# Kernel optimization log

Measured on AMD Instinct MI355X. Metric: run time of the kernel, lower is better.

The kernel has to match this reference:

```python
import jax, jax.numpy as jnp
import numpy as np

NEG_SLOPE = 0.2
EPS = 1e-16


def setup_inputs() -> dict:
    key = jax.random.key(0)
    k1, k2, k3, k4, k5 = jax.random.split(key, 5)
    N, E, F_IN, H, C = 100000, 1600000, 128, 4, 32
    x = jax.random.normal(k1, (N, F_IN), dtype=jnp.float32)
    edge_index = jax.random.randint(k2, (2, E), 0, N, dtype=jnp.int64)
    W = jax.random.normal(k3, (F_IN, H * C), dtype=jnp.float32) * (1.0 / np.sqrt(F_IN))
    att_src = jax.random.normal(k4, (H, C), dtype=jnp.float32) * 0.1
    att_dst = jax.random.normal(k5, (H, C), dtype=jnp.float32) * 0.1
    bias = jnp.zeros((H * C,), dtype=jnp.float32)
    return {"x": x, "edge_index": edge_index, "W": W, "att_src": att_src,
            "att_dst": att_dst, "bias": bias}


def reference(x, edge_index, W, att_src, att_dst, bias):
    N = x.shape[0]
    H, C = att_src.shape
    # PyG GATConv default: add self-loops
    loops = jnp.arange(N, dtype=edge_index.dtype)
    src = jnp.concatenate([edge_index[0], loops])  # [E+N]
    dst = jnp.concatenate([edge_index[1], loops])  # [E+N]

    h = (x @ W).reshape(N, H, C)                  # [N,H,C]
    a_src = jnp.einsum('nhc,hc->nh', h, att_src)  # [N,H]
    a_dst = jnp.einsum('nhc,hc->nh', h, att_dst)  # [N,H]

    e = a_src[src] + a_dst[dst]                   # [E',H]
    e = jax.nn.leaky_relu(e, NEG_SLOPE)

    # segment softmax over destination nodes (numerically stable)
    m = jax.ops.segment_max(e, dst, num_segments=N)      # [N,H]
    p = jnp.exp(e - m[dst])                               # [E',H]
    s = jax.ops.segment_sum(p, dst, num_segments=N)       # [N,H]
    alpha = p / (s[dst] + EPS)                             # [E',H]

    msg = h[src] * alpha[:, :, None]                       # [E',H,C]
    out = jax.ops.segment_sum(msg, dst, num_segments=N)   # [N,H,C]
    return out.reshape(N, H * C) + bias
```

## Files before the change

kernel.cpp:

```cpp
#include <hip/hip_runtime.h>
#include <stdint.h>


#define SLOT 64
#define CNTS 16
#define BCNS 16
#define BCAP 1536
#define MAXB 2048
#define KCH  8192
#define PST  68

typedef __attribute__((ext_vector_type(8))) _Float16 h8;
typedef __attribute__((ext_vector_type(4))) float    f4x;
typedef __attribute__((ext_vector_type(2))) unsigned u32x2;

__device__ __forceinline__ float b2f(unsigned short u) {
    union { unsigned int i; float f; } v; v.i = ((unsigned int)u) << 16; return v.f;
}
__device__ __forceinline__ unsigned short f2b(float f) {
    union { float f; unsigned int i; } v; v.f = f;
    unsigned int i = v.i;
    unsigned int r = (i + 0x7FFFu + ((i >> 16) & 1u)) >> 16;
    return (unsigned short)r;
}
__device__ __forceinline__ unsigned short f2h(float f) {
    union { _Float16 h; unsigned short u; } v; v.h = (_Float16)f; return v.u;
}
__device__ __forceinline__ float h2f(unsigned short u) {
    union { _Float16 h; unsigned short u; } v; v.u = u; return (float)v.h;
}

__global__ void k_detect(const int* __restrict__ eidx, const unsigned int* __restrict__ xw,
                         int* flags) {
    __shared__ int nz, bf;
    if (threadIdx.x == 0) { nz = 0; bf = 0; }
    __syncthreads();
    int bad = 0;
    for (int i = threadIdx.x; i < 1024; i += 256)
        if (eidx[2 * i + 1] != 0) bad = 1;
    if (bad) atomicOr(&nz, 1);
    int hits = 0;
    for (int i = threadIdx.x; i < 4096; i += 256) {
        unsigned int e = (xw[i] >> 7) & 0xFFu;
        if (e >= 0x60u && e < 0xA0u) ++hits;
    }
    atomicAdd(&bf, hits);
    __syncthreads();
    if (threadIdx.x == 0) {
        flags[0] = (nz == 0) ? 1 : 0;
        flags[1] = (bf > 3072) ? 1 : 0;
    }
}

__device__ __forceinline__ int edge_at(const int* idx32, const long long* idx64,
                                       int is64, long long pos) {
    return is64 ? (int)idx64[pos] : idx32[pos];
}

__global__ void k_prep(const void* __restrict__ Wv, const void* __restrict__ asv,
                       const void* __restrict__ adv, const void* __restrict__ bv,
                       const int* __restrict__ flags,
                       _Float16* __restrict__ Wth, _Float16* __restrict__ Wtl,
                       float* __restrict__ attf , float* __restrict__ biasf ) {
    int isbf = flags[1];
    int tid = blockIdx.x * 256 + threadIdx.x;
    for (int i = tid; i < 16384; i += gridDim.x * 256) {
        int col = i >> 7, k = i & 127;
        float w = isbf ? b2f(((const unsigned short*)Wv)[k * 128 + col])
                       : ((const float*)Wv)[k * 128 + col];
        unsigned short hi = f2h(w);
        unsigned short lo = f2h(w - h2f(hi));
        ((unsigned short*)Wth)[i] = hi;
        ((unsigned short*)Wtl)[i] = lo;
    }
    if (blockIdx.x == 0) {
        for (int i = threadIdx.x; i < 128; i += 256) {
            attf[i]       = isbf ? b2f(((const unsigned short*)asv)[i]) : ((const float*)asv)[i];
            attf[128 + i] = isbf ? b2f(((const unsigned short*)adv)[i]) : ((const float*)adv)[i];
            biasf[i]      = isbf ? b2f(((const unsigned short*)bv)[i]) : ((const float*)bv)[i];
        }
    }
}

__global__ __launch_bounds__(256) void k_gemm_scatter(
    const void* __restrict__ xv,
    const _Float16* __restrict__ Wth, const _Float16* __restrict__ Wtl,
    const float* __restrict__ attf, const int* __restrict__ flags,
    unsigned short* __restrict__ hbf, float* __restrict__ asf,
    float* __restrict__ adf, int N,
    const int* __restrict__ idx32, const long long* __restrict__ idx64,
    int* __restrict__ bcnt, unsigned* __restrict__ bdat,
    int* __restrict__ cnt, int* __restrict__ esrc,
    int E, int Gg, int SB) {
    __shared__ unsigned short xsh[64 * 128];
    __shared__ unsigned short xsl[64 * 128];
    int tid = threadIdx.x;
    int bid = blockIdx.x;

    if (bid < SB) {
        int is64 = flags[0];
        int NBK = (N + 63) >> 6;
        long long e0 = (long long)bid * KCH;
        long long e1 = e0 + KCH; if (e1 > E) e1 = E;
        if (e0 >= E) return;

        if (NBK <= MAXB) {
            int wid = tid >> 6;
            int* h0 = (int*)xsh; int* h1 = h0 + MAXB;
            int* h2 = (int*)xsl; int* h3 = h2 + MAXB;
            int* hw = (wid == 0) ? h0 : (wid == 1) ? h1 : (wid == 2) ? h2 : h3;
            for (int i = tid; i < NBK; i += 256) { h0[i] = 0; h1[i] = 0; h2[i] = 0; h3[i] = 0; }
            __syncthreads();
            for (long long e = e0 + tid; e < e1; e += 256) {
                int d = is64 ? (int)idx64[(long long)E + e] : idx32[E + e];
                atomicAdd(&hw[d >> 6], 1);
            }
            __syncthreads();
            for (int b = tid; b < NBK; b += 256) {
                int c0 = h0[b], c1 = h1[b], c2 = h2[b], c3 = h3[b];
                int t = c0 + c1 + c2 + c3;
                int base = (t > 0) ? atomicAdd(&bcnt[(size_t)b * BCNS], t) : 0;
                h0[b] = base;
                h1[b] = base + c0;
                h2[b] = base + c0 + c1;
                h3[b] = base + c0 + c1 + c2;
            }
            __syncthreads();
            for (long long e = e0 + tid; e < e1; e += 256) {
                int d, s;
                if (is64) {
                    d = (int)idx64[(long long)E + e]; s = (int)idx64[e];
                } else {
                    d = idx32[E + e]; s = idx32[e];
                }
                int b = d >> 6;
                int p = atomicAdd(&hw[b], 1);
                if (p < BCAP)
                    bdat[(size_t)b * BCAP + p] = (unsigned)s | ((unsigned)(d & 63) << 26);
            }
        } else {
            for (long long e = e0 + tid; e < e1; e += 256) {
                int d = edge_at(idx32, idx64, is64, (long long)E + e);
                int s = edge_at(idx32, idx64, is64, e);
                int p = atomicAdd(&cnt[(size_t)d * CNTS], 1);
                if (p < SLOT) esrc[(size_t)d * SLOT + p] = s;
            }
        }
        return;
    }

    int rb = bid - SB;
    if (rb >= Gg) return;
    int r0 = rb * 64;
    int isbf = flags[1];
    int w = tid >> 6;
    int lane = tid & 63;
    int li = lane & 15;
    int g  = lane >> 4;
    int c0 = w * 32;

    h8 Bh[2][4], Bl[2][4];
#pragma unroll
    for (int t = 0; t < 2; ++t)
#pragma unroll
        for (int s = 0; s < 4; ++s) {
            size_t o = (size_t)(c0 + 16 * t + li) * 128 + 32 * s + 8 * g;
            Bh[t][s] = *(const h8*)(Wth + o);
            Bl[t][s] = *(const h8*)(Wtl + o);
        }

#pragma unroll
    for (int it = 0; it < 4; ++it) {
        int idx = it * 2048 + tid * 8;
        int r = idx >> 7, k = idx & 127;
        int gr = r0 + r; if (gr >= N) gr = N - 1;
        float v[8];
        if (isbf) {
            uint4 raw = *(const uint4*)((const unsigned short*)xv + (size_t)gr * 128 + k);
            v[0] = b2f((unsigned short)(raw.x & 0xFFFFu)); v[1] = b2f((unsigned short)(raw.x >> 16));
            v[2] = b2f((unsigned short)(raw.y & 0xFFFFu)); v[3] = b2f((unsigned short)(raw.y >> 16));
            v[4] = b2f((unsigned short)(raw.z & 0xFFFFu)); v[5] = b2f((unsigned short)(raw.z >> 16));
            v[6] = b2f((unsigned short)(raw.w & 0xFFFFu)); v[7] = b2f((unsigned short)(raw.w >> 16));
        } else {
            const float* xf = (const float*)xv;
            float4 a = *(const float4*)(xf + (size_t)gr * 128 + k);
            float4 b = *(const float4*)(xf + (size_t)gr * 128 + k + 4);
            v[0] = a.x; v[1] = a.y; v[2] = a.z; v[3] = a.w;
            v[4] = b.x; v[5] = b.y; v[6] = b.z; v[7] = b.w;
        }
        uint4 PH, PL;
        unsigned int ph[4], pl[4];
#pragma unroll
        for (int jj = 0; jj < 4; ++jj) {
            unsigned short h0 = f2h(v[2 * jj]), h1 = f2h(v[2 * jj + 1]);
            unsigned short l0 = f2h(v[2 * jj] - h2f(h0));
            unsigned short l1 = f2h(v[2 * jj + 1] - h2f(h1));
            ph[jj] = (unsigned int)h0 | ((unsigned int)h1 << 16);
            pl[jj] = (unsigned int)l0 | ((unsigned int)l1 << 16);
        }
        PH.x = ph[0]; PH.y = ph[1]; PH.z = ph[2]; PH.w = ph[3];
        PL.x = pl[0]; PL.y = pl[1]; PL.z = pl[2]; PL.w = pl[3];
        int off = r * 256 + ((2 * k) ^ ((r & 7) << 4));
        *(uint4*)((char*)xsh + off) = PH;
        *(uint4*)((char*)xsl + off) = PL;
    }
    __syncthreads();

    f4x acc[4][2];
#pragma unroll
    for (int m = 0; m < 4; ++m)
#pragma unroll
        for (int t = 0; t < 2; ++t) acc[m][t] = (f4x){0.f, 0.f, 0.f, 0.f};

#pragma unroll
    for (int s = 0; s < 4; ++s) {
#pragma unroll
        for (int m = 0; m < 4; ++m) {
            int row = 16 * m + li;
            int kb = (32 * s + 8 * g) * 2;
            int off = row * 256 + (kb ^ ((row & 7) << 4));
            h8 ah = *(const h8*)((const char*)xsh + off);
            h8 al = *(const h8*)((const char*)xsl + off);
#pragma unroll
            for (int t = 0; t < 2; ++t) {
                acc[m][t] = __builtin_amdgcn_mfma_f32_16x16x32_f16(ah, Bh[t][s], acc[m][t], 0, 0, 0);
                acc[m][t] = __builtin_amdgcn_mfma_f32_16x16x32_f16(al, Bh[t][s], acc[m][t], 0, 0, 0);
                acc[m][t] = __builtin_amdgcn_mfma_f32_16x16x32_f16(ah, Bl[t][s], acc[m][t], 0, 0, 0);
            }
        }
    }

    float at_s0 = attf[c0 + li],       at_s1 = attf[c0 + 16 + li];
    float at_d0 = attf[128 + c0 + li], at_d1 = attf[128 + c0 + 16 + li];
#pragma unroll
    for (int m = 0; m < 4; ++m) {
        float s1v[4], s2v[4];
#pragma unroll
        for (int j = 0; j < 4; ++j) {
            s1v[j] = acc[m][0][j] * at_s0 + acc[m][1][j] * at_s1;
            s2v[j] = acc[m][0][j] * at_d0 + acc[m][1][j] * at_d1;
        }
#pragma unroll
        for (int j = 0; j < 4; ++j) {
#pragma unroll
            for (int msk = 1; msk < 16; msk <<= 1) {
                s1v[j] += __shfl_xor(s1v[j], msk);
                s2v[j] += __shfl_xor(s2v[j], msk);
            }
        }
        if (li == 0) {
#pragma unroll
            for (int j = 0; j < 4; ++j) {
                int gr = r0 + 16 * m + 4 * g + j;
                if (gr < N) {
                    asf[(size_t)gr * 4 + w] = s1v[j];
                    adf[(size_t)gr * 4 + w] = s2v[j];
                }
            }
        }
    }

    __syncthreads();
#pragma unroll
    for (int m = 0; m < 4; ++m)
#pragma unroll
        for (int t = 0; t < 2; ++t)
#pragma unroll
            for (int j = 0; j < 4; ++j)
                xsh[(16 * m + 4 * g + j) * 128 + c0 + 16 * t + li] = f2b(acc[m][t][j]);
    __syncthreads();
#pragma unroll
    for (int it = 0; it < 4; ++it) {
        int u = it * 2048 + tid * 8;
        int r = u >> 7, k = u & 127;
        int gr = r0 + r;
        if (gr < N)
            *(uint4*)(hbf + (size_t)gr * 128 + k) = *(const uint4*)(xsh + u);
    }
}

template <int NB>
__device__ __forceinline__ void agg_node2(
    int n, int dl, int deg, int lane,
    const int lslot[64][SLOT], float* psh,
    const unsigned short* __restrict__ hbf,
    const float* __restrict__ asf, const float* __restrict__ adf,
    float a[4], float& invho) {
    int half = lane >> 5;
    int cl = lane & 31;
    int hd = cl >> 3;
    int sl = (lane == 0) ? n : ((lane <= deg) ? lslot[dl][lane - 1] : n);
    float4 av, adv;
    asm volatile("global_load_dwordx4 %0, %1, off"
                 : "=v"(av) : "v"((const void*)(asf + (size_t)sl * 4)));
    asm volatile("global_load_dwordx4 %0, %1, off"
                 : "=v"(adv) : "v"((const void*)(adf + (size_t)n * 4)));
    u32x2 vv[NB * 8];
#pragma unroll
    for (int k = 0; k < NB * 8; ++k) {
        int it = 2 * k + half;
        int s = (it == 0) ? n : ((it <= deg) ? lslot[dl][it - 1] : n);
        asm volatile("global_load_dwordx2 %0, %1, off"
                     : "=v"(vv[k]) : "v"((const void*)(hbf + (size_t)s * 128 + 4 * cl)));
    }
    asm volatile("s_waitcnt vmcnt(%0)" :: "n"(NB * 8));
    __builtin_amdgcn_sched_barrier(0);

    float p0 = 0.f, p1 = 0.f, p2 = 0.f, p3 = 0.f;
    if (lane <= deg) {
        float e0 = av.x + adv.x; e0 = fmaxf(e0, 0.2f * e0); p0 = __expf(e0);
        float e1 = av.y + adv.y; e1 = fmaxf(e1, 0.2f * e1); p1 = __expf(e1);
        float e2 = av.z + adv.z; e2 = fmaxf(e2, 0.2f * e2); p2 = __expf(e2);
        float e3 = av.w + adv.w; e3 = fmaxf(e3, 0.2f * e3); p3 = __expf(e3);
    }
    psh[0 * PST + lane] = p0; psh[1 * PST + lane] = p1;
    psh[2 * PST + lane] = p2; psh[3 * PST + lane] = p3;
    __builtin_amdgcn_wave_barrier();
    asm volatile("s_waitcnt lgkmcnt(0)" ::: "memory");
    __builtin_amdgcn_wave_barrier();

    float ps0 = p0, ps1 = p1, ps2 = p2, ps3 = p3;
#pragma unroll
    for (int m = 1; m < 64; m <<= 1) {
        ps0 += __shfl_xor(ps0, m);
        ps1 += __shfl_xor(ps1, m);
        ps2 += __shfl_xor(ps2, m);
        ps3 += __shfl_xor(ps3, m);
    }
    float den = hd == 0 ? ps0 : hd == 1 ? ps1 : hd == 2 ? ps2 : ps3;
    invho = 1.0f / (den + 1e-16f);

#pragma unroll
    for (int bi = 0; bi < NB; ++bi) {
        asm volatile("s_waitcnt vmcnt(%0)" :: "n"(8 * (NB - 1 - bi)));
        __builtin_amdgcn_sched_barrier(0);
#pragma unroll
        for (int k2 = 0; k2 < 8; ++k2) {
            int it = 2 * (bi * 8 + k2) + half;
            float q = psh[hd * PST + it];
            u32x2 v = vv[bi * 8 + k2];
            a[0] += q * b2f((unsigned short)v[0]);
            a[1] += q * b2f((unsigned short)(v[0] >> 16));
            a[2] += q * b2f((unsigned short)v[1]);
            a[3] += q * b2f((unsigned short)(v[1] >> 16));
        }
    }
}

__global__ __launch_bounds__(256) void k_bagg(
    const unsigned* __restrict__ bdat, const int* __restrict__ bcnt,
    const unsigned short* __restrict__ hbf,
    const float* __restrict__ asf, const float* __restrict__ adf,
    const int* __restrict__ idx32, const long long* __restrict__ idx64,
    const float* __restrict__ biasf, const int* __restrict__ flags,
    void* __restrict__ outv, int N, int E) {
    __shared__ int   lcnt[64];
    __shared__ int   lslot[64][SLOT];
    __shared__ float p_all[4][4 * PST];
    int b = blockIdx.x, tid = threadIdx.x;
    int wid = tid >> 6, lane = tid & 63, head = lane >> 4;

    if (tid < 64) lcnt[tid] = 0;
    __syncthreads();
    int mm = bcnt[(size_t)b * BCNS];
    int ovf = (mm > BCAP);
    if (mm > BCAP) mm = BCAP;
    for (int i = tid; i < mm; i += 256) {
        unsigned e = bdat[(size_t)b * BCAP + i];
        int dl = (int)(e >> 26);
        int p = atomicAdd(&lcnt[dl], 1);
        if (p < SLOT) lslot[dl][p] = (int)(e & 0x03FFFFFFu);
    }
    __syncthreads();

    int cl = lane & 31;
    float b0 = biasf[2 * lane], b1 = biasf[2 * lane + 1];
    float4 bq4 = *(const float4*)(biasf + 4 * cl);
    float* psh = p_all[wid];
    int isbf = flags[1];
    int is64 = flags[0];

    for (int u = 0; u < 16; ++u) {
        int dl = wid * 16 + u;
        int n = (b << 6) + dl;
        if (n >= N) break;
        int deg = lcnt[dl];
        bool fb = ovf || (deg > SLOT - 1);

        if (!fb && deg <= 31) {
            float a4[4] = {0.f, 0.f, 0.f, 0.f};
            float invh = 0.f;
            int nb = (deg + 16) >> 4;
            if (nb == 1) agg_node2<1>(n, dl, deg, lane, lslot, psh, hbf, asf, adf, a4, invh);
            else         agg_node2<2>(n, dl, deg, lane, lslot, psh, hbf, asf, adf, a4, invh);
#pragma unroll
            for (int c = 0; c < 4; ++c) a4[c] += __shfl_xor(a4[c], 32);
            float o0 = a4[0] * invh + bq4.x, o1 = a4[1] * invh + bq4.y;
            float o2 = a4[2] * invh + bq4.z, o3 = a4[3] * invh + bq4.w;
            if (lane < 32) {
                if (isbf) {
                    u32x2 pk;
                    pk[0] = (unsigned)f2b(o0) | ((unsigned)f2b(o1) << 16);
                    pk[1] = (unsigned)f2b(o2) | ((unsigned)f2b(o3) << 16);
                    *(u32x2*)((unsigned*)outv + (size_t)n * 64 + cl * 2) = pk;
                } else {
                    float4 f4v; f4v.x = o0; f4v.y = o1; f4v.z = o2; f4v.w = o3;
                    *(float4*)((float*)outv + (size_t)n * 128 + cl * 4) = f4v;
                }
            }
        } else if (!fb) {
            float a0 = 0.f, a1 = 0.f;
            float4 adv = *(const float4*)(adf + (size_t)n * 4);
            int sl = (lane == 0) ? n : ((lane <= deg) ? lslot[dl][lane - 1] : n);
            float4 av = *(const float4*)(asf + (size_t)sl * 4);
            float p0 = 0.f, p1 = 0.f, p2 = 0.f, p3 = 0.f;
            if (lane <= deg) {
                float e0 = av.x + adv.x; e0 = fmaxf(e0, 0.2f * e0); p0 = __expf(e0);
                float e1 = av.y + adv.y; e1 = fmaxf(e1, 0.2f * e1); p1 = __expf(e1);
                float e2 = av.z + adv.z; e2 = fmaxf(e2, 0.2f * e2); p2 = __expf(e2);
                float e3 = av.w + adv.w; e3 = fmaxf(e3, 0.2f * e3); p3 = __expf(e3);
            }
            psh[0 * PST + lane] = p0; psh[1 * PST + lane] = p1;
            psh[2 * PST + lane] = p2; psh[3 * PST + lane] = p3;
            __builtin_amdgcn_wave_barrier();
            asm volatile("s_waitcnt lgkmcnt(0)" ::: "memory");
            __builtin_amdgcn_wave_barrier();
            float ps0 = p0, ps1 = p1, ps2 = p2, ps3 = p3;
#pragma unroll
            for (int m = 1; m < 64; m <<= 1) {
                ps0 += __shfl_xor(ps0, m);
                ps1 += __shfl_xor(ps1, m);
                ps2 += __shfl_xor(ps2, m);
                ps3 += __shfl_xor(ps3, m);
            }
            float den = head == 0 ? ps0 : head == 1 ? ps1 : head == 2 ? ps2 : ps3;
            float invh = 1.0f / (den + 1e-16f);
            int nb = (deg + 8) >> 3;
            for (int bi = 0; bi < nb; ++bi) {
                unsigned vt[8];
#pragma unroll
                for (int k2 = 0; k2 < 8; ++k2) {
                    int it = bi * 8 + k2;
                    int s = (it == 0) ? n : ((it <= deg) ? lslot[dl][it - 1] : n);
                    vt[k2] = *(const unsigned int*)(hbf + (size_t)s * 128 + 2 * lane);
                }
#pragma unroll
                for (int k2 = 0; k2 < 8; ++k2) {
                    float q = psh[head * PST + bi * 8 + k2];
                    a0 += q * b2f((unsigned short)vt[k2]);
                    a1 += q * b2f((unsigned short)(vt[k2] >> 16));
                }
            }
            a0 = a0 * invh + b0;
            a1 = a1 * invh + b1;
            if (isbf) {
                unsigned int pk = (unsigned int)f2b(a0) | ((unsigned int)f2b(a1) << 16);
                ((unsigned int*)outv)[(size_t)n * 64 + lane] = pk;
            } else {
                float2 f2; f2.x = a0; f2.y = a1;
                *(float2*)((float*)outv + (size_t)n * 128 + 2 * lane) = f2;
            }
        } else {
            float a0 = 0.f, a1 = 0.f;
            float4 adv = *(const float4*)(adf + (size_t)n * 4);
            float adh = head == 0 ? adv.x : head == 1 ? adv.y : head == 2 ? adv.z : adv.w;
            float den = 0.f;
            {
                float ev = asf[(size_t)n * 4 + head] + adh; ev = fmaxf(ev, 0.2f * ev);
                float p = __expf(ev);
                unsigned int v = *(const unsigned int*)(hbf + (size_t)n * 128 + 2 * lane);
                den += p;
                a0 += p * b2f((unsigned short)v);
                a1 += p * b2f((unsigned short)(v >> 16));
            }
            for (int e = 0; e < E; ++e) {
                int d = edge_at(idx32, idx64, is64, (long long)E + e);
                if (d == n) {
                    int s = edge_at(idx32, idx64, is64, e);
                    float ev = asf[(size_t)s * 4 + head] + adh; ev = fmaxf(ev, 0.2f * ev);
                    float p = __expf(ev);
                    unsigned int v = *(const unsigned int*)(hbf + (size_t)s * 128 + 2 * lane);
                    den += p;
                    a0 += p * b2f((unsigned short)v);
                    a1 += p * b2f((unsigned short)(v >> 16));
                }
            }
            float invh = 1.0f / (den + 1e-16f);
            a0 = a0 * invh + b0;
            a1 = a1 * invh + b1;
            if (isbf) {
                unsigned int pk = (unsigned int)f2b(a0) | ((unsigned int)f2b(a1) << 16);
                ((unsigned int*)outv)[(size_t)n * 64 + lane] = pk;
            } else {
                float2 f2; f2.x = a0; f2.y = a1;
                *(float2*)((float*)outv + (size_t)n * 128 + 2 * lane) = f2;
            }
        }
        __builtin_amdgcn_wave_barrier();
    }
}

__global__ __launch_bounds__(256) void k_aggregate(
    const unsigned short* __restrict__ hbf,
    const float* __restrict__ asf, const float* __restrict__ adf,
    const int* __restrict__ cnt, const int* __restrict__ esrc,
    const int* __restrict__ idx32, const long long* __restrict__ idx64,
    const float* __restrict__ biasf, const int* __restrict__ flags,
    void* __restrict__ outv, int N, int E) {
    __shared__ float p_sh_all[4][SLOT * 4];
    __shared__ int   s_sh_all[4][SLOT];
    int wid = threadIdx.x >> 6;
    int lane = threadIdx.x & 63;
    int n = blockIdx.x * 4 + wid;
    if (n >= N) n = N - 1;
    float* p_sh = p_sh_all[wid];
    int*   s_sh = s_sh_all[wid];
    int head = lane >> 4;

    int deg = cnt[(size_t)n * CNTS];
    float4 adv = *(const float4*)(adf + (size_t)n * 4);
    bool fb = (deg > SLOT - 1);

    float p0 = 0.f, p1 = 0.f, p2 = 0.f, p3 = 0.f;
    if (!fb && lane <= deg) {
        int s = (lane == 0) ? n : esrc[(size_t)n * SLOT + lane - 1];
        float4 av = *(const float4*)(asf + (size_t)s * 4);
        float e0 = av.x + adv.x; e0 = fmaxf(e0, 0.2f * e0); p0 = __expf(e0);
        float e1 = av.y + adv.y; e1 = fmaxf(e1, 0.2f * e1); p1 = __expf(e1);
        float e2 = av.z + adv.z; e2 = fmaxf(e2, 0.2f * e2); p2 = __expf(e2);
        float e3 = av.w + adv.w; e3 = fmaxf(e3, 0.2f * e3); p3 = __expf(e3);
        s_sh[lane] = s;
        p_sh[lane * 4 + 0] = p0; p_sh[lane * 4 + 1] = p1;
        p_sh[lane * 4 + 2] = p2; p_sh[lane * 4 + 3] = p3;
    }
    __syncthreads();

    float b0 = biasf[2 * lane], b1 = biasf[2 * lane + 1];
    float a0 = 0.f, a1 = 0.f, invh;

    if (!fb) {
        float ps0 = p0, ps1 = p1, ps2 = p2, ps3 = p3;
#pragma unroll
        for (int m = 1; m < 64; m <<= 1) {
            ps0 += __shfl_xor(ps0, m);
            ps1 += __shfl_xor(ps1, m);
            ps2 += __shfl_xor(ps2, m);
            ps3 += __shfl_xor(ps3, m);
        }
        float den = head == 0 ? ps0 : head == 1 ? ps1 : head == 2 ? ps2 : ps3;
        invh = 1.0f / (den + 1e-16f);

        int tot = deg + 1;
        int i = 0;
        for (; i + 3 < tot; i += 4) {
            int s0 = s_sh[i], s1 = s_sh[i + 1], s2 = s_sh[i + 2], s3 = s_sh[i + 3];
            float q0 = p_sh[i * 4 + head],       q1 = p_sh[(i + 1) * 4 + head];
            float q2 = p_sh[(i + 2) * 4 + head], q3 = p_sh[(i + 3) * 4 + head];
            unsigned int v0 = *(const unsigned int*)(hbf + (size_t)s0 * 128 + 2 * lane);
            unsigned int v1 = *(const unsigned int*)(hbf + (size_t)s1 * 128 + 2 * lane);
            unsigned int v2 = *(const unsigned int*)(hbf + (size_t)s2 * 128 + 2 * lane);
            unsigned int v3 = *(const unsigned int*)(hbf + (size_t)s3 * 128 + 2 * lane);
            a0 += q0 * b2f((unsigned short)v0) + q1 * b2f((unsigned short)v1)
                + q2 * b2f((unsigned short)v2) + q3 * b2f((unsigned short)v3);
            a1 += q0 * b2f((unsigned short)(v0 >> 16)) + q1 * b2f((unsigned short)(v1 >> 16))
                + q2 * b2f((unsigned short)(v2 >> 16)) + q3 * b2f((unsigned short)(v3 >> 16));
        }
        for (; i < tot; ++i) {
            int s0 = s_sh[i];
            float q0 = p_sh[i * 4 + head];
            unsigned int v0 = *(const unsigned int*)(hbf + (size_t)s0 * 128 + 2 * lane);
            a0 += q0 * b2f((unsigned short)v0);
            a1 += q0 * b2f((unsigned short)(v0 >> 16));
        }
    } else {
        int is64 = flags[0];
        float adh = head == 0 ? adv.x : head == 1 ? adv.y : head == 2 ? adv.z : adv.w;
        float den = 0.f;
        {
            float ev = asf[(size_t)n * 4 + head] + adh; ev = fmaxf(ev, 0.2f * ev);
            float p = __expf(ev);
            unsigned int v = *(const unsigned int*)(hbf + (size_t)n * 128 + 2 * lane);
            den += p;
            a0 += p * b2f((unsigned short)v);
            a1 += p * b2f((unsigned short)(v >> 16));
        }
        for (int e = 0; e < E; ++e) {
            int d = edge_at(idx32, idx64, is64, (long long)E + e);
            if (d == n) {
                int s = edge_at(idx32, idx64, is64, e);
                float ev = asf[(size_t)s * 4 + head] + adh; ev = fmaxf(ev, 0.2f * ev);
                float p = __expf(ev);
                unsigned int v = *(const unsigned int*)(hbf + (size_t)s * 128 + 2 * lane);
                den += p;
                a0 += p * b2f((unsigned short)v);
                a1 += p * b2f((unsigned short)(v >> 16));
            }
        }
        invh = 1.0f / (den + 1e-16f);
    }

    a0 = a0 * invh + b0;
    a1 = a1 * invh + b1;
    if (flags[1]) {
        unsigned int pk = (unsigned int)f2b(a0) | ((unsigned int)f2b(a1) << 16);
        ((unsigned int*)outv)[(size_t)n * 64 + lane] = pk;
    } else {
        float2 f2; f2.x = a0; f2.y = a1;
        *(float2*)((float*)outv + (size_t)n * 128 + 2 * lane) = f2;
    }
}

extern "C" void kernel_launch(void* const* d_in, const int* in_sizes, int n_in,
                              void* d_out, int out_size, void* d_ws, size_t ws_size,
                              hipStream_t stream) {
    const void*      xv    = d_in[0];
    const int*       idx32 = (const int*)d_in[1];
    const long long* idx64 = (const long long*)d_in[1];

    int N = in_sizes[0] / 128;
    int E = in_sizes[1] / 2;

    char* ws = (char*)d_ws;
    size_t o = 0;
    auto alloc = [&](size_t bytes) {
        size_t r = o; o += (bytes + 255) & ~(size_t)255; return r;
    };
    unsigned short* hbf = (unsigned short*)(ws + alloc((size_t)N * 128 * 2));
    _Float16* Wth = (_Float16*)(ws + alloc(16384 * 2));
    _Float16* Wtl = (_Float16*)(ws + alloc(16384 * 2));
    float* attf  = (float*)(ws + alloc(256 * 4));
    float* biasf = (float*)(ws + alloc(128 * 4));
    float* asf   = (float*)(ws + alloc((size_t)N * 4 * 4));
    float* adf   = (float*)(ws + alloc((size_t)N * 4 * 4));
    int* cnt     = (int*)(ws + alloc((size_t)N * CNTS * 4));
    int* flags   = (int*)(ws + alloc(256));
    int* esrc    = (int*)(ws + alloc((size_t)N * SLOT * 4));
    int NBK = (N + 63) >> 6;
    int* bcnt      = (int*)(ws + alloc((size_t)NBK * BCNS * 4));
    unsigned* bdat = (unsigned*)(ws + alloc((size_t)NBK * BCAP * 4));

    int Gg = (N + 63) / 64;
    int SB = (E + KCH - 1) / KCH;
    int NB = SB + Gg;

    k_detect<<<1, 256, 0, stream>>>(idx32, (const unsigned int*)xv, flags);
    k_prep<<<16, 256, 0, stream>>>(d_in[2], d_in[3], d_in[4], d_in[5], flags, Wth, Wtl, attf, biasf);
    if (NBK <= MAXB) {
        hipMemsetAsync(bcnt, 0, (size_t)NBK * BCNS * 4, stream);
        k_gemm_scatter<<<NB, 256, 0, stream>>>(xv, Wth, Wtl, attf, flags, hbf, asf, adf, N,
                                               idx32, idx64, bcnt, bdat, cnt, esrc, E, Gg, SB);
        k_bagg<<<NBK, 256, 0, stream>>>(bdat, bcnt, hbf, asf, adf, idx32, idx64,
                                        biasf, flags, d_out, N, E);
    } else {
        hipMemsetAsync(cnt, 0, (size_t)N * CNTS * 4, stream);
        k_gemm_scatter<<<NB, 256, 0, stream>>>(xv, Wth, Wtl, attf, flags, hbf, asf, adf, N,
                                               idx32, idx64, bcnt, bdat, cnt, esrc, E, Gg, SB);
        k_aggregate<<<(N + 3) / 4, 256, 0, stream>>>(hbf, asf, adf, cnt, esrc, idx32, idx64,
                                                     biasf, flags, d_out, N, E);
    }
}
```

Measured before the change: 254.0 us.

## Fold detection and bucket-count clearing into prep kernel; split aggregation blocks in two

Merges the dtype/index detection kernel and the bucket-counter memset into the prep kernel, removing two launches from the stream. Each prep block recomputes the bf16 heuristic locally so it does not need a cross-block flag read. The bucket aggregation kernel now launches two blocks per 64-node bucket, each handling 32 destination nodes, which doubles parallelism. The cost is that both blocks redundantly read and bin the whole bucket's edge list into shared memory.

```diff
diff --git a/kernel.cpp b/kernel.cpp
--- a/kernel.cpp
+++ b/kernel.cpp
@@ -30,28 +30,6 @@
     union { _Float16 h; unsigned short u; } v; v.u = u; return (float)v.h;
 }
 
-__global__ void k_detect(const int* __restrict__ eidx, const unsigned int* __restrict__ xw,
-                         int* flags) {
-    __shared__ int nz, bf;
-    if (threadIdx.x == 0) { nz = 0; bf = 0; }
-    __syncthreads();
-    int bad = 0;
-    for (int i = threadIdx.x; i < 1024; i += 256)
-        if (eidx[2 * i + 1] != 0) bad = 1;
-    if (bad) atomicOr(&nz, 1);
-    int hits = 0;
-    for (int i = threadIdx.x; i < 4096; i += 256) {
-        unsigned int e = (xw[i] >> 7) & 0xFFu;
-        if (e >= 0x60u && e < 0xA0u) ++hits;
-    }
-    atomicAdd(&bf, hits);
-    __syncthreads();
-    if (threadIdx.x == 0) {
-        flags[0] = (nz == 0) ? 1 : 0;
-        flags[1] = (bf > 3072) ? 1 : 0;
-    }
-}
-
 __device__ __forceinline__ int edge_at(const int* idx32, const long long* idx64,
                                        int is64, long long pos) {
     return is64 ? (int)idx64[pos] : idx32[pos];
@@ -59,12 +37,37 @@
 
 __global__ void k_prep(const void* __restrict__ Wv, const void* __restrict__ asv,
                        const void* __restrict__ adv, const void* __restrict__ bv,
-                       const int* __restrict__ flags,
+                       const int* __restrict__ eidx, const unsigned int* __restrict__ xw,
+                       int* __restrict__ flags,
                        _Float16* __restrict__ Wth, _Float16* __restrict__ Wtl,
-                       float* __restrict__ attf , float* __restrict__ biasf ) {
-    int isbf = flags[1];
-    int tid = blockIdx.x * 256 + threadIdx.x;
-    for (int i = tid; i < 16384; i += gridDim.x * 256) {
+                       float* __restrict__ attf , float* __restrict__ biasf ,
+                       int* __restrict__ bcnt, int nbcnt ) {
+    __shared__ int nz, bf;
+    int tid = threadIdx.x;
+    if (tid == 0) { nz = 0; bf = 0; }
+    __syncthreads();
+    int hits = 0;
+    for (int i = tid; i < 4096; i += 256) {
+        unsigned int e = (xw[i] >> 7) & 0xFFu;
+        if (e >= 0x60u && e < 0xA0u) ++hits;
+    }
+    atomicAdd(&bf, hits);
+    if (blockIdx.x == 0) {
+        int bad = 0;
+        for (int i = tid; i < 1024; i += 256)
+            if (eidx[2 * i + 1] != 0) bad = 1;
+        if (bad) atomicOr(&nz, 1);
+    }
+    __syncthreads();
+    int isbf = (bf > 3072) ? 1 : 0;
+    if (blockIdx.x == 0 && tid == 0) {
+        flags[0] = (nz == 0) ? 1 : 0;
+        flags[1] = isbf;
+    }
+    for (int i = blockIdx.x * 256 + tid; i < nbcnt; i += gridDim.x * 256)
+        bcnt[i] = 0;
+    int gtid = blockIdx.x * 256 + tid;
+    for (int i = gtid; i < 16384; i += gridDim.x * 256) {
         int col = i >> 7, k = i & 127;
         float w = isbf ? b2f(((const unsigned short*)Wv)[k * 128 + col])
                        : ((const float*)Wv)[k * 128 + col];
@@ -74,7 +77,7 @@
         ((unsigned short*)Wtl)[i] = lo;
     }
     if (blockIdx.x == 0) {
-        for (int i = threadIdx.x; i < 128; i += 256) {
+        for (int i = tid; i < 128; i += 256) {
             attf[i]       = isbf ? b2f(((const unsigned short*)asv)[i]) : ((const float*)asv)[i];
             attf[128 + i] = isbf ? b2f(((const unsigned short*)adv)[i]) : ((const float*)adv)[i];
             biasf[i]      = isbf ? b2f(((const unsigned short*)bv)[i]) : ((const float*)bv)[i];
@@ -357,7 +360,9 @@
     __shared__ int   lcnt[64];
     __shared__ int   lslot[64][SLOT];
     __shared__ float p_all[4][4 * PST];
-    int b = blockIdx.x, tid = threadIdx.x;
+    int b = blockIdx.x >> 1;
+    int bh = blockIdx.x & 1;
+    int tid = threadIdx.x;
     int wid = tid >> 6, lane = tid & 63, head = lane >> 4;
 
     if (tid < 64) lcnt[tid] = 0;
@@ -380,8 +385,8 @@
     int isbf = flags[1];
     int is64 = flags[0];
 
-    for (int u = 0; u < 16; ++u) {
-        int dl = wid * 16 + u;
+    for (int u = 0; u < 8; ++u) {
+        int dl = bh * 32 + wid * 8 + u;
         int n = (b << 6) + dl;
         if (n >= N) break;
         int deg = lcnt[dl];
@@ -643,14 +648,15 @@
     int SB = (E + KCH - 1) / KCH;
     int NB = SB + Gg;
 
-    k_detect<<<1, 256, 0, stream>>>(idx32, (const unsigned int*)xv, flags);
-    k_prep<<<16, 256, 0, stream>>>(d_in[2], d_in[3], d_in[4], d_in[5], flags, Wth, Wtl, attf, biasf);
+    k_prep<<<16, 256, 0, stream>>>(d_in[2], d_in[3], d_in[4], d_in[5],
+                                   idx32, (const unsigned int*)xv, flags,
+                                   Wth, Wtl, attf, biasf,
+                                   bcnt, (NBK <= MAXB) ? NBK * BCNS : 0);
     if (NBK <= MAXB) {
-        hipMemsetAsync(bcnt, 0, (size_t)NBK * BCNS * 4, stream);
         k_gemm_scatter<<<NB, 256, 0, stream>>>(xv, Wth, Wtl, attf, flags, hbf, asf, adf, N,
                                                idx32, idx64, bcnt, bdat, cnt, esrc, E, Gg, SB);
-        k_bagg<<<NBK, 256, 0, stream>>>(bdat, bcnt, hbf, asf, adf, idx32, idx64,
-                                        biasf, flags, d_out, N, E);
+        k_bagg<<<NBK * 2, 256, 0, stream>>>(bdat, bcnt, hbf, asf, adf, idx32, idx64,
+                                            biasf, flags, d_out, N, E);
     } else {
         hipMemsetAsync(cnt, 0, (size_t)N * CNTS * 4, stream);
         k_gemm_scatter<<<NB, 256, 0, stream>>>(xv, Wth, Wtl, attf, flags, hbf, asf, adf, N,
```

New measurement: 253.3 us, median of 2. About the same (-0.3%).
